# Kernel tuning notes

Measured on AMD Instinct MI355X. Metric: run time of the kernel, lower is better.

The kernel has to match this reference:

```python
import jax, jax.numpy as jnp
import numpy as np
import math

S, E, D, H = 2048, 1024, 64, 16  # seq, embedding_dim (=D*H), per-head d_model, heads


def setup_inputs() -> dict:
    ks = jax.random.split(jax.random.key(0), 14)
    u = lambda k, sh: jax.random.uniform(k, sh, dtype=jnp.float32)
    n = lambda k, sh, s=0.02: s * jax.random.normal(k, sh, dtype=jnp.float32)
    return {
        "x": jax.random.normal(ks[0], (S, E), dtype=jnp.float32),
        # nn.Parameter(torch.rand(d_model, embedding_dim))
        "Wk": u(ks[1], (D, E)),
        "Wq": u(ks[2], (D, E)),
        "Wv": u(ks[3], (D, E)),
        # per-head Linear(d_model, d_model): weight [out,in]=[D,D], bias [D]
        "hWk": n(ks[4], (H, D, D)), "hbk": n(ks[5], (H, D)),
        "hWv": n(ks[6], (H, D, D)), "hbv": n(ks[7], (H, D)),
        "hWq": n(ks[8], (H, D, D)), "hbq": n(ks[9], (H, D)),
        # last_linear: Linear(D*H, D*H)
        "Wo": n(ks[10], (E, E)), "bo": n(ks[11], (E,)),
        # LayerNorm(D*H)
        "gamma": jnp.ones((E,), jnp.float32),
        "beta": jnp.zeros((E,), jnp.float32),
    }


def reference(x, Wk, Wq, Wv, hWk, hbk, hWv, hbv, hWq, hbq, Wo, bo, gamma, beta):
    # shared projections: [S, E] @ [E, D] -> [S, D]
    K = x @ Wk.T
    Q = x @ Wq.T
    V = x @ Wv.T
    # per-head linears (torch Linear: y = x @ W.T + b), vectorized over heads
    Kh = jnp.einsum('sd,hed->hse', K, hWk) + hbk[:, None, :]  # [H, S, D]
    Vh = jnp.einsum('sd,hed->hse', V, hWv) + hbv[:, None, :]
    Qh = jnp.einsum('sd,hed->hse', Q, hWq) + hbq[:, None, :]
    # scaled dot product attention; scale uses sqrt(d_model)
    scores = jnp.einsum('hqd,hkd->hqk', Qh, Kh) / math.sqrt(D)  # [H, S, S]
    attn = jax.nn.softmax(scores, axis=-1)
    O = jnp.einsum('hqk,hkd->hqd', attn, Vh)  # [H, S, D]
    # concat heads along feature dim (head order) -> [S, H*D]
    cat = jnp.transpose(O, (1, 0, 2)).reshape(S, H * D)
    out = cat @ Wo.T + bo
    # residual + LayerNorm (eps 1e-5)
    y = out + x
    mu = jnp.mean(y, axis=-1, keepdims=True)
    var = jnp.mean(jnp.square(y - mu), axis=-1, keepdims=True)
    return (y - mu) * jax.lax.rsqrt(var + 1e-5) * gamma + beta
```

## Files before the change

kernel.cpp:

```cpp
#include <hip/hip_runtime.h>
#include <math.h>

#define S 2048
#define E 1024
#define D 64
#define H 16

using f16 = _Float16;
typedef _Float16 v8h __attribute__((ext_vector_type(8)));
typedef _Float16 v4h __attribute__((ext_vector_type(4)));
typedef float v4f __attribute__((ext_vector_type(4)));

__device__ __forceinline__ float fexp2(float x) { return __builtin_amdgcn_exp2f(x); }

__device__ __forceinline__ void glds16(const f16* g, f16* l) {
    __builtin_amdgcn_global_load_lds(
        (const __attribute__((address_space(1))) void*)g,
        (__attribute__((address_space(3))) void*)l, 16, 0, 0);
}

__global__ void prep(const float* __restrict__ x, const float* __restrict__ Wo,
                     const float* __restrict__ hWk, const float* __restrict__ hWq,
                     const float* __restrict__ hWv,
                     const float* __restrict__ Wk, const float* __restrict__ Wq,
                     const float* __restrict__ Wv,
                     f16* __restrict__ Xh, f16* __restrict__ WoB,
                     f16* __restrict__ Wc) {
    __shared__ f16 Ah[64][72];
    __shared__ f16 Bt[64][72];
    const int t = threadIdx.x;

    if (blockIdx.x < 3072) {
        const size_t i = (size_t)blockIdx.x * 256 + t;
        const size_t NX = (size_t)S * E / 4;
        if (i < NX) {
            v4f w = ((const v4f*)x)[i];
            v4h h = {(f16)w[0], (f16)w[1], (f16)w[2], (f16)w[3]};
            ((v4h*)Xh)[i] = h;
        } else {
            const size_t j = i - NX;
            v4f w = ((const v4f*)Wo)[j];
            v4h h = {(f16)w[0], (f16)w[1], (f16)w[2], (f16)w[3]};
            ((v4h*)WoB)[j] = h;
        }
        return;
    }

    const int bb = blockIdx.x - 3072;
    const int th = bb >> 4;
    const int type = th >> 4, h = th & 15;
    const int e0 = (bb & 15) * 64;
    const float* hW = ((type == 0) ? hWk : (type == 1) ? hWq : hWv) + (size_t)h * D * D;
    const float* W  = (type == 0) ? Wk : (type == 1) ? Wq : Wv;

    {
        const int r16 = t >> 4, c4 = (t & 15) * 4;
#pragma unroll
        for (int rep = 0; rep < 4; ++rep) {
            const int row = rep * 16 + r16;
            v4f a = *(const v4f*)&hW[(size_t)row * D + c4];
#pragma unroll
            for (int j = 0; j < 4; ++j) Ah[row][c4 + j] = (f16)a[j];
            v4f w = *(const v4f*)&W[(size_t)row * E + e0 + c4];
#pragma unroll
            for (int j = 0; j < 4; ++j) Bt[c4 + j][row] = (f16)w[j];
        }
    }
    __syncthreads();

    const int wave = t >> 6, lane = t & 63;
    const int quad = lane >> 4, l16 = lane & 15;
    v4f acc[4] = {};
#pragma unroll
    for (int ks = 0; ks < 2; ++ks) {
        v8h af = *(const v8h*)&Ah[wave * 16 + l16][ks * 32 + quad * 8];
#pragma unroll
        for (int nt = 0; nt < 4; ++nt) {
            v8h bf = *(const v8h*)&Bt[nt * 16 + l16][ks * 32 + quad * 8];
            acc[nt] = __builtin_amdgcn_mfma_f32_16x16x32_f16(af, bf, acc[nt], 0, 0, 0);
        }
    }
#pragma unroll
    for (int r = 0; r < 4; ++r) {
        const int e2 = wave * 16 + quad * 4 + r;
#pragma unroll
        for (int nt = 0; nt < 4; ++nt)
            Wc[((size_t)th * D + e2) * E + e0 + nt * 16 + l16] = (f16)acc[nt][r];
    }
}

__global__ __launch_bounds__(256) void qkv_gemm(
        const f16* __restrict__ Xh, const f16* __restrict__ Wc,
        const float* __restrict__ hbk, const float* __restrict__ hbq,
        const float* __restrict__ hbv,
        f16* __restrict__ Kh, f16* __restrict__ Qh, f16* __restrict__ VhT) {
    const int m0 = blockIdx.x * 128;
    const int n0 = blockIdx.y * 64;
    const int type = n0 >> 10, h = (n0 >> 6) & 15;
    const float* hb = ((type == 0) ? hbk : (type == 1) ? hbq : hbv) + h * D;

    const int t = threadIdx.x;
    const int wave = t >> 6, lane = t & 63;
    const int quad = lane >> 4, l16 = lane & 15;
    const int wm = wave >> 1, wn = wave & 1;

    __shared__ f16 As[128 * 64];
    __shared__ f16 Bs[64 * 64];

    v4f acc[4][2] = {};
    const int lrow8 = lane >> 3, lg = lane & 7;

    for (int k0 = 0; k0 < E; k0 += 64) {
        __syncthreads();
#pragma unroll
        for (int jj = 0; jj < 4; ++jj) {
            const int j = wave * 4 + jj;
            const int row = j * 8 + lrow8;
            const int g = lg ^ (row & 7);
            glds16(Xh + (size_t)(m0 + row) * E + k0 + g * 8, &As[j * 512]);
        }
#pragma unroll
        for (int jj = 0; jj < 2; ++jj) {
            const int j = wave * 2 + jj;
            const int row = j * 8 + lrow8;
            const int g = lg ^ (row & 7);
            glds16(Wc + (size_t)(n0 + row) * E + k0 + g * 8, &Bs[j * 512]);
        }
        __syncthreads();

#pragma unroll
        for (int ks = 0; ks < 2; ++ks) {
            v8h a[4], b[2];
#pragma unroll
            for (int mt = 0; mt < 4; ++mt) {
                const int row = wm * 64 + mt * 16 + l16;
                a[mt] = *(const v8h*)&As[row * 64 + (((ks * 4 + quad) ^ (row & 7)) * 8)];
            }
#pragma unroll
            for (int nt = 0; nt < 2; ++nt) {
                const int row = wn * 32 + nt * 16 + l16;
                b[nt] = *(const v8h*)&Bs[row * 64 + (((ks * 4 + quad) ^ (row & 7)) * 8)];
            }
#pragma unroll
            for (int mt = 0; mt < 4; ++mt)
#pragma unroll
                for (int nt = 0; nt < 2; ++nt)
                    acc[mt][nt] = __builtin_amdgcn_mfma_f32_16x16x32_f16(a[mt], b[nt], acc[mt][nt], 0, 0, 0);
        }
    }

    if (type == 2) {
#pragma unroll
        for (int mt = 0; mt < 4; ++mt)
#pragma unroll
            for (int nt = 0; nt < 2; ++nt) {
                const int d = wn * 32 + nt * 16 + l16;
                const int s = m0 + wm * 64 + mt * 16 + quad * 4;
                const float b = hb[d];
                v4h vh;
#pragma unroll
                for (int r = 0; r < 4; ++r) vh[r] = (f16)(acc[mt][nt][r] + b);
                *(v4h*)(VhT + ((size_t)h * D + d) * S + s) = vh;
            }
    } else {
        f16* outp = (type == 0) ? Kh : Qh;
#pragma unroll
        for (int mt = 0; mt < 4; ++mt)
#pragma unroll
            for (int r = 0; r < 4; ++r) {
                const int s = m0 + wm * 64 + mt * 16 + quad * 4 + r;
#pragma unroll
                for (int nt = 0; nt < 2; ++nt) {
                    const int d = wn * 32 + nt * 16 + l16;
                    outp[((size_t)h * S + s) * D + d] = (f16)(acc[mt][nt][r] + hb[d]);
                }
            }
    }
}

#define NSPLIT 4
#define KSPAN (S / NSPLIT)
#define ITERS (KSPAN / 64)
#define PPAD 72

__global__ __launch_bounds__(256, 5) void attn_mfma(
        const f16* __restrict__ Qh, const f16* __restrict__ Kh,
        const f16* __restrict__ VhT, f16* __restrict__ Opart,
        float* __restrict__ ml) {
    const int h = blockIdx.y;
    const int q0 = blockIdx.x * 64;
    const int sp = blockIdx.z;
    const int t = threadIdx.x;
    const int wave = t >> 6, lane = t & 63;
    const int quad = lane >> 4, l16 = lane & 15;

    __shared__ f16 Kt[64 * 64];
    __shared__ f16 Vt[80 * 64];
    __shared__ union { f16 P[4][16][PPAD]; f16 O[64][PPAD]; } PO;

    {
        v4h one = {(f16)1, (f16)1, (f16)1, (f16)1};
        *(v4h*)&Vt[64 * 64 + t * 4] = one;
    }

    const int qrow = q0 + wave * 16 + l16;
    v8h qf[2];
    {
        const v8h* qp = (const v8h*)(Qh + ((size_t)h * S + qrow) * D);
        qf[0] = qp[quad];
        qf[1] = qp[quad + 4];
    }

    v4f oc[5] = {};
    float m_run = -INFINITY;
    const float scale = 0.125f * 1.44269504f;
    const int kb = sp * KSPAN;
    const int srow = lane >> 3, sg = lane & 7;

    for (int it = 0; it < ITERS; ++it) {
        __syncthreads();
#pragma unroll
        for (int half = 0; half < 2; ++half) {
            const int row = wave * 16 + half * 8 + srow;
            const int g = sg ^ (row & 7);
            glds16(Kh + ((size_t)h * S + kb + it * 64 + row) * D + g * 8,
                   &Kt[(wave * 16 + half * 8) * 64]);
            glds16(VhT + ((size_t)h * D + row) * S + kb + it * 64 + g * 8,
                   &Vt[(wave * 16 + half * 8) * 64]);
        }
        __syncthreads();

        v4f sc[4] = {};
#pragma unroll
        for (int ks = 0; ks < 2; ++ks)
#pragma unroll
            for (int mt = 0; mt < 4; ++mt) {
                const int key = mt * 16 + l16;
                v8h kf = *(const v8h*)&Kt[key * 64 + (((ks * 4 + quad) ^ (key & 7)) * 8)];
                sc[mt] = __builtin_amdgcn_mfma_f32_16x16x32_f16(kf, qf[ks], sc[mt], 0, 0, 0);
            }

        float v = sc[0][0];
#pragma unroll
        for (int mt = 0; mt < 4; ++mt)
#pragma unroll
            for (int r = 0; r < 4; ++r) v = fmaxf(v, sc[mt][r]);
        v = fmaxf(v, __shfl_xor(v, 16));
        v = fmaxf(v, __shfl_xor(v, 32));
        v *= scale;
        const float mnew = fmaxf(m_run, v);
        const float alpha = fexp2(m_run - mnew);
        m_run = mnew;
#pragma unroll
        for (int i = 0; i < 5; ++i) oc[i] *= alpha;

#pragma unroll
        for (int mt = 0; mt < 4; ++mt) {
            const float p0 = fexp2(fmaf(sc[mt][0], scale, -mnew));
            const float p1 = fexp2(fmaf(sc[mt][1], scale, -mnew));
            const float p2 = fexp2(fmaf(sc[mt][2], scale, -mnew));
            const float p3 = fexp2(fmaf(sc[mt][3], scale, -mnew));
            auto lo = __builtin_amdgcn_cvt_pkrtz(p0, p1);
            auto hi = __builtin_amdgcn_cvt_pkrtz(p2, p3);
            v4h ph; ph[0] = lo[0]; ph[1] = lo[1]; ph[2] = hi[0]; ph[3] = hi[1];
            *(v4h*)&PO.P[wave][l16][mt * 16 + quad * 4] = ph;
        }

#pragma unroll
        for (int ks = 0; ks < 2; ++ks) {
            v8h pf = *(const v8h*)&PO.P[wave][l16][ks * 32 + quad * 8];
#pragma unroll
            for (int mt = 0; mt < 5; ++mt) {
                const int dr = mt * 16 + l16;
                v8h vf = *(const v8h*)&Vt[dr * 64 + (((ks * 4 + quad) ^ (dr & 7)) * 8)];
                oc[mt] = __builtin_amdgcn_mfma_f32_16x16x32_f16(vf, pf, oc[mt], 0, 0, 0);
            }
        }
    }

    const float l = oc[4][0];
    const float invl = 1.f / l;
    __syncthreads();
#pragma unroll
    for (int mt = 0; mt < 4; ++mt) {
        auto lo = __builtin_amdgcn_cvt_pkrtz(oc[mt][0] * invl, oc[mt][1] * invl);
        auto hi = __builtin_amdgcn_cvt_pkrtz(oc[mt][2] * invl, oc[mt][3] * invl);
        v4h oh; oh[0] = lo[0]; oh[1] = lo[1]; oh[2] = hi[0]; oh[3] = hi[1];
        *(v4h*)&PO.O[wave * 16 + l16][mt * 16 + quad * 4] = oh;
    }
    if (quad == 0) {
        float* mlp = ml + (((size_t)sp * H + h) * S + qrow) * 2;
        mlp[0] = m_run;
        mlp[1] = l;
    }
    __syncthreads();
    {
        const int q = t >> 2, dg = (t & 3) * 16;
        v8h o0 = *(const v8h*)&PO.O[q][dg];
        v8h o1 = *(const v8h*)&PO.O[q][dg + 8];
        f16* dst = Opart + (((size_t)sp * H + h) * S + q0 + q) * D + dg;
        *(v8h*)dst = o0;
        *(v8h*)(dst + 8) = o1;
    }
}

__global__ void attn_combine(const f16* __restrict__ Opart,
                             const float* __restrict__ ml,
                             f16* __restrict__ cat) {
    const int q = blockIdx.x;
    const int t = threadIdx.x;
#pragma unroll
    for (int i = 0; i < 4; ++i) {
        const int idx = i * 256 + t;
        const int h = idx >> 6, d = idx & 63;
        float m[NSPLIT], lv[NSPLIT];
        float M = -INFINITY;
#pragma unroll
        for (int sp = 0; sp < NSPLIT; ++sp) {
            const float* mlp = ml + (((size_t)sp * H + h) * S + q) * 2;
            m[sp] = mlp[0]; lv[sp] = mlp[1];
            M = fmaxf(M, m[sp]);
        }
        float asum = 0.f, o = 0.f;
#pragma unroll
        for (int sp = 0; sp < NSPLIT; ++sp) {
            const float a = fexp2(m[sp] - M) * lv[sp];
            asum += a;
            o += a * (float)Opart[(((size_t)sp * H + h) * S + q) * D + d];
        }
        cat[(size_t)q * E + h * D + d] = (f16)(o / asum);
    }
}

__global__ __launch_bounds__(256) void gemm_y(
        const f16* __restrict__ cat, const f16* __restrict__ WoB,
        const float* __restrict__ bo, const float* __restrict__ x,
        float* __restrict__ y) {
    const int m0 = blockIdx.x * 64;
    const int n0 = blockIdx.y * 64;
    const int t = threadIdx.x;
    const int wave = t >> 6, lane = t & 63;
    const int quad = lane >> 4, l16 = lane & 15;
    const int wm = wave >> 1, wn = wave & 1;

    __shared__ f16 As[64 * 64];
    __shared__ f16 Bs[64 * 64];

    v4f acc[2][2] = {};
    const int lrow8 = lane >> 3, lg = lane & 7;

    for (int k0 = 0; k0 < E; k0 += 64) {
        __syncthreads();
#pragma unroll
        for (int jj = 0; jj < 2; ++jj) {
            const int j = wave * 2 + jj;
            const int row = j * 8 + lrow8;
            const int g = lg ^ (row & 7);
            glds16(cat + (size_t)(m0 + row) * E + k0 + g * 8, &As[j * 512]);
            glds16(WoB + (size_t)(n0 + row) * E + k0 + g * 8, &Bs[j * 512]);
        }
        __syncthreads();

#pragma unroll
        for (int ks = 0; ks < 2; ++ks) {
            v8h a[2], b[2];
#pragma unroll
            for (int mt = 0; mt < 2; ++mt) {
                const int row = wm * 32 + mt * 16 + l16;
                a[mt] = *(const v8h*)&As[row * 64 + (((ks * 4 + quad) ^ (row & 7)) * 8)];
            }
#pragma unroll
            for (int nt = 0; nt < 2; ++nt) {
                const int row = wn * 32 + nt * 16 + l16;
                b[nt] = *(const v8h*)&Bs[row * 64 + (((ks * 4 + quad) ^ (row & 7)) * 8)];
            }
#pragma unroll
            for (int mt = 0; mt < 2; ++mt)
#pragma unroll
                for (int nt = 0; nt < 2; ++nt)
                    acc[mt][nt] = __builtin_amdgcn_mfma_f32_16x16x32_f16(a[mt], b[nt], acc[mt][nt], 0, 0, 0);
        }
    }

#pragma unroll
    for (int mt = 0; mt < 2; ++mt)
#pragma unroll
        for (int r = 0; r < 4; ++r) {
            const int m = m0 + wm * 32 + mt * 16 + quad * 4 + r;
#pragma unroll
            for (int nt = 0; nt < 2; ++nt) {
                const int e = n0 + wn * 32 + nt * 16 + l16;
                y[(size_t)m * E + e] = acc[mt][nt][r] + bo[e] + x[(size_t)m * E + e];
            }
        }
}

__global__ void ln(const float* __restrict__ y,
                   const float* __restrict__ gamma,
                   const float* __restrict__ beta,
                   float* __restrict__ out) {
    const int s = blockIdx.x;
    const int t = threadIdx.x;
    __shared__ float red[256];

    v4f yv = *(const v4f*)(y + (size_t)s * E + t * 4);
    red[t] = yv[0] + yv[1] + yv[2] + yv[3];
    __syncthreads();
    for (int w = 128; w > 0; w >>= 1) {
        if (t < w) red[t] += red[t + w];
        __syncthreads();
    }
    const float mu = red[0] * (1.f / E);
    __syncthreads();

    float lv = 0.f;
#pragma unroll
    for (int i = 0; i < 4; ++i) { float dd = yv[i] - mu; lv += dd * dd; }
    red[t] = lv;
    __syncthreads();
    for (int w = 128; w > 0; w >>= 1) {
        if (t < w) red[t] += red[t + w];
        __syncthreads();
    }
    const float rstd = rsqrtf(red[0] * (1.f / E) + 1e-5f);

    v4f o;
#pragma unroll
    for (int i = 0; i < 4; ++i) {
        const int e = t * 4 + i;
        o[i] = (yv[i] - mu) * rstd * gamma[e] + beta[e];
    }
    *(v4f*)(out + (size_t)s * E + t * 4) = o;
}

extern "C" void kernel_launch(void* const* d_in, const int* in_sizes, int n_in,
                              void* d_out, int out_size, void* d_ws, size_t ws_size,
                              hipStream_t stream) {
    const float* x     = (const float*)d_in[0];
    const float* Wk    = (const float*)d_in[1];
    const float* Wq    = (const float*)d_in[2];
    const float* Wv    = (const float*)d_in[3];
    const float* hWk   = (const float*)d_in[4];
    const float* hbk   = (const float*)d_in[5];
    const float* hWv   = (const float*)d_in[6];
    const float* hbv   = (const float*)d_in[7];
    const float* hWq   = (const float*)d_in[8];
    const float* hbq   = (const float*)d_in[9];
    const float* Wo    = (const float*)d_in[10];
    const float* bo    = (const float*)d_in[11];
    const float* gamma = (const float*)d_in[12];
    const float* beta  = (const float*)d_in[13];
    float* out = (float*)d_out;

    char* base = (char*)d_ws;
    const size_t MB = 1u << 20;
    f16*   Kh    = (f16*)(base);
    f16*   Qh    = (f16*)(base + 4 * MB);
    f16*   VhT   = (f16*)(base + 8 * MB);
    f16*   Opart = (f16*)(base + 12 * MB);
    float* ml    = (float*)(base + 28 * MB);
    f16*   WoB   = (f16*)(base + 29 * MB);
    f16*   Xh    = (f16*)(base + 31 * MB);
    f16*   Wc    = (f16*)(base + 35 * MB);
    f16*   cat   = (f16*)(base + 41 * MB);
    float* y     = (float*)(base + 45 * MB);

    prep<<<3072 + 768, 256, 0, stream>>>(x, Wo, hWk, hWq, hWv, Wk, Wq, Wv,
                                         Xh, WoB, Wc);
    qkv_gemm<<<dim3(S / 128, 3 * H * D / 64), 256, 0, stream>>>(Xh, Wc, hbk, hbq, hbv,
                                                                Kh, Qh, VhT);
    attn_mfma<<<dim3(S / 64, H, NSPLIT), 256, 0, stream>>>(Qh, Kh, VhT, Opart, ml);
    attn_combine<<<S, 256, 0, stream>>>(Opart, ml, cat);
    gemm_y<<<dim3(S / 64, E / 64), 256, 0, stream>>>(cat, WoB, bo, x, y);
    ln<<<S, 256, 0, stream>>>(y, gamma, beta, out);
}
```

Before: 166.9 us.

## Fold softmax scale into Q, vectorize combine, and store residual output in fp16

Pre-multiplies Q by the softmax scale times log2(e) in the QKV epilogue, which drops the per-score multiply in attention. The row-max reduction becomes a tree instead of a serial chain. The split-combine kernel now handles four contiguous elements per thread with vector loads and stores. The output GEMM reads the fp16 copy of x for the residual and writes y in fp16, halving its traffic to the LayerNorm kernel, at the cost of precision in the residual and pre-norm values.

```diff
diff --git a/kernel.cpp b/kernel.cpp
--- a/kernel.cpp
+++ b/kernel.cpp
@@ -10,6 +10,8 @@
 typedef _Float16 v8h __attribute__((ext_vector_type(8)));
 typedef _Float16 v4h __attribute__((ext_vector_type(4)));
 typedef float v4f __attribute__((ext_vector_type(4)));
+
+#define QSCALE (0.125f * 1.44269504f)
 
 __device__ __forceinline__ float fexp2(float x) { return __builtin_amdgcn_exp2f(x); }
 
@@ -164,6 +166,7 @@
             }
     } else {
         f16* outp = (type == 0) ? Kh : Qh;
+        const float osc = (type == 1) ? QSCALE : 1.f;
 #pragma unroll
         for (int mt = 0; mt < 4; ++mt)
 #pragma unroll
@@ -172,7 +175,7 @@
 #pragma unroll
                 for (int nt = 0; nt < 2; ++nt) {
                     const int d = wn * 32 + nt * 16 + l16;
-                    outp[((size_t)h * S + s) * D + d] = (f16)(acc[mt][nt][r] + hb[d]);
+                    outp[((size_t)h * S + s) * D + d] = (f16)((acc[mt][nt][r] + hb[d]) * osc);
                 }
             }
     }
@@ -213,7 +216,6 @@
 
     v4f oc[5] = {};
     float m_run = -INFINITY;
-    const float scale = 0.125f * 1.44269504f;
     const int kb = sp * KSPAN;
     const int srow = lane >> 3, sg = lane & 7;
 
@@ -240,14 +242,15 @@
                 sc[mt] = __builtin_amdgcn_mfma_f32_16x16x32_f16(kf, qf[ks], sc[mt], 0, 0, 0);
             }
 
-        float v = sc[0][0];
-#pragma unroll
-        for (int mt = 0; mt < 4; ++mt)
-#pragma unroll
-            for (int r = 0; r < 4; ++r) v = fmaxf(v, sc[mt][r]);
+        float a0 = fmaxf(sc[0][0], sc[0][1]), a1 = fmaxf(sc[0][2], sc[0][3]);
+        float a2 = fmaxf(sc[1][0], sc[1][1]), a3 = fmaxf(sc[1][2], sc[1][3]);
+        float a4 = fmaxf(sc[2][0], sc[2][1]), a5 = fmaxf(sc[2][2], sc[2][3]);
+        float a6 = fmaxf(sc[3][0], sc[3][1]), a7 = fmaxf(sc[3][2], sc[3][3]);
+        float b0 = fmaxf(a0, a1), b1 = fmaxf(a2, a3);
+        float b2 = fmaxf(a4, a5), b3 = fmaxf(a6, a7);
+        float v = fmaxf(fmaxf(b0, b1), fmaxf(b2, b3));
         v = fmaxf(v, __shfl_xor(v, 16));
         v = fmaxf(v, __shfl_xor(v, 32));
-        v *= scale;
         const float mnew = fmaxf(m_run, v);
         const float alpha = fexp2(m_run - mnew);
         m_run = mnew;
@@ -256,10 +259,10 @@
 
 #pragma unroll
         for (int mt = 0; mt < 4; ++mt) {
-            const float p0 = fexp2(fmaf(sc[mt][0], scale, -mnew));
-            const float p1 = fexp2(fmaf(sc[mt][1], scale, -mnew));
-            const float p2 = fexp2(fmaf(sc[mt][2], scale, -mnew));
-            const float p3 = fexp2(fmaf(sc[mt][3], scale, -mnew));
+            const float p0 = fexp2(sc[mt][0] - mnew);
+            const float p1 = fexp2(sc[mt][1] - mnew);
+            const float p2 = fexp2(sc[mt][2] - mnew);
+            const float p3 = fexp2(sc[mt][3] - mnew);
             auto lo = __builtin_amdgcn_cvt_pkrtz(p0, p1);
             auto hi = __builtin_amdgcn_cvt_pkrtz(p2, p3);
             v4h ph; ph[0] = lo[0]; ph[1] = lo[1]; ph[2] = hi[0]; ph[3] = hi[1];
@@ -309,33 +312,38 @@
                              f16* __restrict__ cat) {
     const int q = blockIdx.x;
     const int t = threadIdx.x;
-#pragma unroll
-    for (int i = 0; i < 4; ++i) {
-        const int idx = i * 256 + t;
-        const int h = idx >> 6, d = idx & 63;
-        float m[NSPLIT], lv[NSPLIT];
-        float M = -INFINITY;
-#pragma unroll
-        for (int sp = 0; sp < NSPLIT; ++sp) {
-            const float* mlp = ml + (((size_t)sp * H + h) * S + q) * 2;
-            m[sp] = mlp[0]; lv[sp] = mlp[1];
-            M = fmaxf(M, m[sp]);
-        }
-        float asum = 0.f, o = 0.f;
-#pragma unroll
-        for (int sp = 0; sp < NSPLIT; ++sp) {
-            const float a = fexp2(m[sp] - M) * lv[sp];
-            asum += a;
-            o += a * (float)Opart[(((size_t)sp * H + h) * S + q) * D + d];
-        }
-        cat[(size_t)q * E + h * D + d] = (f16)(o / asum);
-    }
+    const int idx = t * 4;
+    const int h = idx >> 6, d0 = idx & 63;
+
+    float m[NSPLIT], lv[NSPLIT];
+    float M = -INFINITY;
+#pragma unroll
+    for (int sp = 0; sp < NSPLIT; ++sp) {
+        const float* mlp = ml + (((size_t)sp * H + h) * S + q) * 2;
+        m[sp] = mlp[0]; lv[sp] = mlp[1];
+        M = fmaxf(M, m[sp]);
+    }
+    float asum = 0.f;
+    float o[4] = {0.f, 0.f, 0.f, 0.f};
+#pragma unroll
+    for (int sp = 0; sp < NSPLIT; ++sp) {
+        const float a = fexp2(m[sp] - M) * lv[sp];
+        asum += a;
+        v4h op = *(const v4h*)(Opart + (((size_t)sp * H + h) * S + q) * D + d0);
+#pragma unroll
+        for (int j = 0; j < 4; ++j) o[j] += a * (float)op[j];
+    }
+    const float inv = 1.f / asum;
+    v4h co;
+#pragma unroll
+    for (int j = 0; j < 4; ++j) co[j] = (f16)(o[j] * inv);
+    *(v4h*)(cat + (size_t)q * E + idx) = co;
 }
 
 __global__ __launch_bounds__(256) void gemm_y(
         const f16* __restrict__ cat, const f16* __restrict__ WoB,
-        const float* __restrict__ bo, const float* __restrict__ x,
-        float* __restrict__ y) {
+        const float* __restrict__ bo, const f16* __restrict__ Xh,
+        f16* __restrict__ y) {
     const int m0 = blockIdx.x * 64;
     const int n0 = blockIdx.y * 64;
     const int t = threadIdx.x;
@@ -390,12 +398,13 @@
 #pragma unroll
             for (int nt = 0; nt < 2; ++nt) {
                 const int e = n0 + wn * 32 + nt * 16 + l16;
-                y[(size_t)m * E + e] = acc[mt][nt][r] + bo[e] + x[(size_t)m * E + e];
-            }
-        }
-}
-
-__global__ void ln(const float* __restrict__ y,
+                y[(size_t)m * E + e] =
+                    (f16)(acc[mt][nt][r] + bo[e] + (float)Xh[(size_t)m * E + e]);
+            }
+        }
+}
+
+__global__ void ln(const f16* __restrict__ y,
                    const float* __restrict__ gamma,
                    const float* __restrict__ beta,
                    float* __restrict__ out) {
@@ -403,7 +412,11 @@
     const int t = threadIdx.x;
     __shared__ float red[256];
 
-    v4f yv = *(const v4f*)(y + (size_t)s * E + t * 4);
+    v4h yh = *(const v4h*)(y + (size_t)s * E + t * 4);
+    float yv[4];
+#pragma unroll
+    for (int i = 0; i < 4; ++i) yv[i] = (float)yh[i];
+
     red[t] = yv[0] + yv[1] + yv[2] + yv[3];
     __syncthreads();
     for (int w = 128; w > 0; w >>= 1) {
@@ -463,7 +476,7 @@
     f16*   Xh    = (f16*)(base + 31 * MB);
     f16*   Wc    = (f16*)(base + 35 * MB);
     f16*   cat   = (f16*)(base + 41 * MB);
-    float* y     = (float*)(base + 45 * MB);
+    f16*   y     = (f16*)(base + 45 * MB);
 
     prep<<<3072 + 768, 256, 0, stream>>>(x, Wo, hWk, hWq, hWv, Wk, Wq, Wv,
                                          Xh, WoB, Wc);
@@ -471,6 +484,6 @@
                                                                 Kh, Qh, VhT);
     attn_mfma<<<dim3(S / 64, H, NSPLIT), 256, 0, stream>>>(Qh, Kh, VhT, Opart, ml);
     attn_combine<<<S, 256, 0, stream>>>(Opart, ml, cat);
-    gemm_y<<<dim3(S / 64, E / 64), 256, 0, stream>>>(cat, WoB, bo, x, y);
+    gemm_y<<<dim3(S / 64, E / 64), 256, 0, stream>>>(cat, WoB, bo, Xh, y);
     ln<<<S, 256, 0, stream>>>(y, gamma, beta, out);
 }
```

New measurement: 170.1 us. Within noise of the previous version (+1.9%).
